# Kernel tuning notes

Measured on AMD Instinct MI355X. Metric: run time of the kernel, lower is better.

Reference implementation:

```python
import jax, jax.numpy as jnp
import numpy as np

INDIM = 1024
OUTDIM = 1024
NNZ = 65536  # expander pattern: avg degree 64 per output row
N = 50000


def setup_inputs() -> dict:
    key = jax.random.key(0)
    k1, k2, k3, k4, k5 = jax.random.split(key, 5)
    x = jax.random.normal(k1, (N, INDIM), dtype=jnp.float32)
    # glorot init for nnz values as in reset_parameters('glorot')
    stdv = np.sqrt(6.0 / (INDIM + OUTDIM))
    nnz_weight = jax.random.uniform(k2, (NNZ,), dtype=jnp.float32, minval=-stdv, maxval=stdv)
    bias = jax.random.normal(k3, (OUTDIM,), dtype=jnp.float32) * 0.02
    row = jax.random.randint(k4, (NNZ,), 0, OUTDIM, dtype=jnp.int64)
    col = jax.random.randint(k5, (NNZ,), 0, INDIM, dtype=jnp.int64)
    edge_index = jnp.stack([row, col])  # [2, NNZ]
    return {"x": x, "nnz_weight": nnz_weight, "bias": bias, "edge_index": edge_index}


def reference(x, nnz_weight, bias, edge_index):
    # SparseTensor(row, col, sizes=(outdim, indim), value=nnz_weight);
    # y = (W @ x^T)^T + bias  ==  x @ W^T + bias
    # Sparsity pattern is fixed & small (1024x1024): scatter values into a
    # dense weight then use a dense GEMM (duplicates accumulate, matching SpMM).
    row, col = edge_index[0], edge_index[1]
    W = jnp.zeros((OUTDIM, INDIM), dtype=nnz_weight.dtype).at[row, col].add(nnz_weight)
    return x @ W.T + bias  # [N, OUTDIM]
```

## Files before the change

kernel.cpp:

```cpp
#include <hip/hip_runtime.h>
#include <cstdint>

#define INDIM 1024
#define OUTDIM 1024
#define NNZ 65536
#define M_ROWS 50000

typedef __bf16 bf16x8 __attribute__((ext_vector_type(8)));
typedef float f32x4 __attribute__((ext_vector_type(4)));
typedef unsigned int u32x4 __attribute__((ext_vector_type(4)));

__global__ void scatter_w_kernel(const float* __restrict__ vals,
                                 const int* __restrict__ edge,
                                 float* __restrict__ Wf) {
    int e = blockIdx.x * blockDim.x + threadIdx.x;
    if (e < NNZ) {
        int r = edge[e];
        int c = edge[NNZ + e];
        atomicAdd(&Wf[r * INDIM + c], vals[e]);
    }
}

__global__ void cvt_w_kernel(const float* __restrict__ Wf,
                             unsigned short* __restrict__ Wb) {
    int i = blockIdx.x * blockDim.x + threadIdx.x;
    unsigned u = __builtin_bit_cast(unsigned, Wf[i]) + 0x8000u;
    Wb[i] = (unsigned short)(u >> 16);
}

__device__ __forceinline__ unsigned pack_bf16x2(float a, float b) {
    unsigned ua = __builtin_bit_cast(unsigned, a) + 0x8000u;
    unsigned ub = __builtin_bit_cast(unsigned, b) + 0x8000u;
    return (ua >> 16) | (ub & 0xffff0000u);
}

__device__ __forceinline__ void async_copy16(const void* g, void* l) {
    __builtin_amdgcn_global_load_lds(
        (const __attribute__((address_space(1))) void*)g,
        (__attribute__((address_space(3))) void*)l, 16, 0, 0);
}

__global__ void __launch_bounds__(256)
gemm_bt_kernel(const float* __restrict__ X,
               const unsigned short* __restrict__ Wb,
               const float* __restrict__ bias,
               float* __restrict__ out) {
    __shared__ unsigned As[128 * 16];
    __shared__ unsigned short Bs[128 * 32];

    const int t = threadIdx.x;
    const int w = t >> 6;
    const int l = t & 63;
    const int wr = w >> 1;
    const int wc = w & 1;
    const int quad = l >> 4;
    const int lr = l & 15;

    const int bid = blockIdx.x;
    int m_t, n_t;
    if (bid < 3072) {
        m_t = ((bid >> 6) << 3) + (bid & 7);
        n_t = (bid >> 3) & 7;
    } else {
        int r = bid - 3072;
        m_t = 384 + (r >> 3);
        n_t = r & 7;
    }
    const int m0 = m_t * 128;
    const int n0 = n_t * 128;

    const int ar  = t >> 1;
    const int ac0 = (t & 1) * 2;
    const int as_sw = (ar >> 1) & 3;
    int arow = m0 + ar;
    if (arow >= M_ROWS) arow = M_ROWS - 1;
    const float* aptr = X + (long)arow * INDIM + (t & 1) * 16;
    unsigned* as_row = &As[ar * 16];
    const int aph0 = (ac0 ^ as_sw) * 4;
    const int aph1 = ((ac0 + 1) ^ as_sw) * 4;

    f32x4 acc[4][4];
#pragma unroll
    for (int i = 0; i < 4; i++)
#pragma unroll
        for (int j = 0; j < 4; j++) acc[i][j] = (f32x4)0.0f;

    float biasv[4];
#pragma unroll
    for (int j = 0; j < 4; j++) biasv[j] = bias[n0 + wc * 64 + j * 16 + lr];

    int bsrc_off[2];
    int brow_[2];
#pragma unroll
    for (int i = 0; i < 2; i++) {
        int c_idx = i * 256 + t;
        int brow = c_idx >> 2;
        int pphys = c_idx & 3;
        int pdata = pphys ^ ((brow >> 1) & 3);
        brow_[i] = brow;
        bsrc_off[i] = pdata * 8;
    }

    for (int kt = 0; kt < INDIM; kt += 32) {
#pragma unroll
        for (int i = 0; i < 2; i++) {
            const unsigned short* g = Wb + (long)(n0 + brow_[i]) * INDIM + kt + bsrc_off[i];
            char* lbase = (char*)Bs + (size_t)(i * 256 + w * 64) * 16;
            async_copy16(g, lbase);
        }

        const float* ap = aptr + kt;
        f32x4 f0 = *(const f32x4*)(ap);
        f32x4 f1 = *(const f32x4*)(ap + 4);
        f32x4 f2 = *(const f32x4*)(ap + 8);
        f32x4 f3 = *(const f32x4*)(ap + 12);
        u32x4 p0, p1;
        p0.x = pack_bf16x2(f0.x, f0.y);
        p0.y = pack_bf16x2(f0.z, f0.w);
        p0.z = pack_bf16x2(f1.x, f1.y);
        p0.w = pack_bf16x2(f1.z, f1.w);
        p1.x = pack_bf16x2(f2.x, f2.y);
        p1.y = pack_bf16x2(f2.z, f2.w);
        p1.z = pack_bf16x2(f3.x, f3.y);
        p1.w = pack_bf16x2(f3.z, f3.w);
        *(u32x4*)(as_row + aph0) = p0;
        *(u32x4*)(as_row + aph1) = p1;

        __syncthreads();

        bf16x8 af[4], bf[4];
#pragma unroll
        for (int i = 0; i < 4; i++) {
            int row = wr * 64 + i * 16 + lr;
            int ph = quad ^ ((row >> 1) & 3);
            af[i] = *(const bf16x8*)((const unsigned short*)As + row * 32 + ph * 8);
        }
#pragma unroll
        for (int j = 0; j < 4; j++) {
            int row = wc * 64 + j * 16 + lr;
            int ph = quad ^ ((row >> 1) & 3);
            bf[j] = *(const bf16x8*)(Bs + row * 32 + ph * 8);
        }
#pragma unroll
        for (int i = 0; i < 4; i++)
#pragma unroll
            for (int j = 0; j < 4; j++)
                acc[i][j] = __builtin_amdgcn_mfma_f32_16x16x32_bf16(af[i], bf[j], acc[i][j], 0, 0, 0);

        __syncthreads();
    }

#pragma unroll
    for (int i = 0; i < 4; i++) {
#pragma unroll
        for (int j = 0; j < 4; j++) {
            int col = n0 + wc * 64 + j * 16 + lr;
#pragma unroll
            for (int r = 0; r < 4; r++) {
                int row = m0 + wr * 64 + i * 16 + quad * 4 + r;
                if (row < M_ROWS) {
                    out[(long)row * OUTDIM + col] = acc[i][j][r] + biasv[j];
                }
            }
        }
    }
}

extern "C" void kernel_launch(void* const* d_in, const int* in_sizes, int n_in,
                              void* d_out, int out_size, void* d_ws, size_t ws_size,
                              hipStream_t stream) {
    const float* x    = (const float*)d_in[0];
    const float* nnzw = (const float*)d_in[1];
    const float* bias = (const float*)d_in[2];
    const int* edge   = (const int*)d_in[3];
    float* out        = (float*)d_out;

    float* Wf         = (float*)d_ws;
    unsigned short* Wb = (unsigned short*)((char*)d_ws + (size_t)OUTDIM * INDIM * 4);

    hipMemsetAsync(Wf, 0, (size_t)OUTDIM * INDIM * sizeof(float), stream);

    scatter_w_kernel<<<NNZ / 256, 256, 0, stream>>>(nnzw, edge, Wf);
    cvt_w_kernel<<<(OUTDIM * INDIM) / 256, 256, 0, stream>>>(Wf, Wb);

    gemm_bt_kernel<<<dim3(3128), 256, 0, stream>>>(x, Wb, bias, out);
}
```

Baseline: 519.8 us.

## Pre-convert X to bf16 and stream both GEMM operands via async LDS loads

Adds a separate pass that converts the fp32 input X to bf16 in workspace memory. The GEMM then loads both A and B tiles with direct global-to-LDS async copies instead of doing per-tile fp32 loads, packing and LDS stores in registers. This removes repeated conversion work from the GEMM and halves the A-operand bytes it reads, and it sets a higher occupancy hint. The cost is an extra full pass that reads X once in fp32 and writes it back in bf16. The new path runs only when the workspace is large enough, otherwise the old kernel is used.

```diff
diff --git a/kernel.cpp b/kernel.cpp
--- a/kernel.cpp
+++ b/kernel.cpp
@@ -34,10 +34,124 @@
     return (ua >> 16) | (ub & 0xffff0000u);
 }
 
+__global__ void cvt_x_kernel(const float* __restrict__ X,
+                             unsigned short* __restrict__ Xb) {
+    long i = ((long)blockIdx.x * blockDim.x + threadIdx.x) * 8;
+    f32x4 a = *(const f32x4*)(X + i);
+    f32x4 b = *(const f32x4*)(X + i + 4);
+    u32x4 p;
+    p.x = pack_bf16x2(a.x, a.y);
+    p.y = pack_bf16x2(a.z, a.w);
+    p.z = pack_bf16x2(b.x, b.y);
+    p.w = pack_bf16x2(b.z, b.w);
+    *(u32x4*)(Xb + i) = p;
+}
+
 __device__ __forceinline__ void async_copy16(const void* g, void* l) {
     __builtin_amdgcn_global_load_lds(
         (const __attribute__((address_space(1))) void*)g,
         (__attribute__((address_space(3))) void*)l, 16, 0, 0);
+}
+
+__global__ void __launch_bounds__(256, 4)
+gemm_bb_kernel(const unsigned short* __restrict__ Xb,
+               const unsigned short* __restrict__ Wb,
+               const float* __restrict__ bias,
+               float* __restrict__ out) {
+    __shared__ unsigned short As[128 * 32];
+    __shared__ unsigned short Bs[128 * 32];
+
+    const int t = threadIdx.x;
+    const int w = t >> 6;
+    const int l = t & 63;
+    const int wr = w >> 1;
+    const int wc = w & 1;
+    const int quad = l >> 4;
+    const int lr = l & 15;
+
+    const int bid = blockIdx.x;
+    int m_t, n_t;
+    if (bid < 3072) {
+        m_t = ((bid >> 6) << 3) + (bid & 7);
+        n_t = (bid >> 3) & 7;
+    } else {
+        int r = bid - 3072;
+        m_t = 384 + (r >> 3);
+        n_t = r & 7;
+    }
+    const int m0 = m_t * 128;
+    const int n0 = n_t * 128;
+
+    int row_[2], soff_[2], arow_[2];
+#pragma unroll
+    for (int i = 0; i < 2; i++) {
+        int c_idx = i * 256 + t;
+        int row = c_idx >> 2;
+        int pphys = c_idx & 3;
+        int pdata = pphys ^ ((row >> 1) & 3);
+        row_[i] = row;
+        soff_[i] = pdata * 8;
+        int ar = m0 + row;
+        arow_[i] = (ar < M_ROWS) ? ar : (M_ROWS - 1);
+    }
+
+    f32x4 acc[4][4];
+#pragma unroll
+    for (int i = 0; i < 4; i++)
+#pragma unroll
+        for (int j = 0; j < 4; j++) acc[i][j] = (f32x4)0.0f;
+
+    float biasv[4];
+#pragma unroll
+    for (int j = 0; j < 4; j++) biasv[j] = bias[n0 + wc * 64 + j * 16 + lr];
+
+    for (int kt = 0; kt < INDIM; kt += 32) {
+#pragma unroll
+        for (int i = 0; i < 2; i++) {
+            async_copy16(Xb + (long)arow_[i] * INDIM + kt + soff_[i],
+                         (char*)As + (size_t)(i * 256 + w * 64) * 16);
+            async_copy16(Wb + (long)(n0 + row_[i]) * INDIM + kt + soff_[i],
+                         (char*)Bs + (size_t)(i * 256 + w * 64) * 16);
+        }
+
+        __syncthreads();
+
+        bf16x8 af[4], bfr[4];
+#pragma unroll
+        for (int i = 0; i < 4; i++) {
+            int row = wr * 64 + i * 16 + lr;
+            int ph = quad ^ ((row >> 1) & 3);
+            af[i] = *(const bf16x8*)(As + row * 32 + ph * 8);
+        }
+#pragma unroll
+        for (int j = 0; j < 4; j++) {
+            int row = wc * 64 + j * 16 + lr;
+            int ph = quad ^ ((row >> 1) & 3);
+            bfr[j] = *(const bf16x8*)(Bs + row * 32 + ph * 8);
+        }
+#pragma unroll
+        for (int i = 0; i < 4; i++)
+#pragma unroll
+            for (int j = 0; j < 4; j++)
+                acc[i][j] = __builtin_amdgcn_mfma_f32_16x16x32_bf16(af[i], bfr[j], acc[i][j], 0, 0, 0);
+
+        __syncthreads();
+    }
+
+#pragma unroll
+    for (int i = 0; i < 4; i++) {
+#pragma unroll
+        for (int j = 0; j < 4; j++) {
+            int col = n0 + wc * 64 + j * 16 + lr;
+#pragma unroll
+            for (int r = 0; r < 4; r++) {
+                int row = m0 + wr * 64 + i * 16 + quad * 4 + r;
+                if (row < M_ROWS) {
+                    out[(long)row * OUTDIM + col] = acc[i][j][r] + biasv[j];
+                }
+            }
+        }
+    }
 }
 
 __global__ void __launch_bounds__(256)
@@ -128,7 +242,7 @@
 
         __syncthreads();
 
-        bf16x8 af[4], bf[4];
+        bf16x8 af[4], bfr[4];
 #pragma unroll
         for (int i = 0; i < 4; i++) {
             int row = wr * 64 + i * 16 + lr;
@@ -139,13 +253,13 @@
         for (int j = 0; j < 4; j++) {
             int row = wc * 64 + j * 16 + lr;
             int ph = quad ^ ((row >> 1) & 3);
-            bf[j] = *(const bf16x8*)(Bs + row * 32 + ph * 8);
+            bfr[j] = *(const bf16x8*)(Bs + row * 32 + ph * 8);
         }
 #pragma unroll
         for (int i = 0; i < 4; i++)
 #pragma unroll
             for (int j = 0; j < 4; j++)
-                acc[i][j] = __builtin_amdgcn_mfma_f32_16x16x32_bf16(af[i], bf[j], acc[i][j], 0, 0, 0);
+                acc[i][j] = __builtin_amdgcn_mfma_f32_16x16x32_bf16(af[i], bfr[j], acc[i][j], 0, 0, 0);
 
         __syncthreads();
     }
@@ -175,13 +289,24 @@
     const int* edge   = (const int*)d_in[3];
     float* out        = (float*)d_out;
 
-    float* Wf         = (float*)d_ws;
-    unsigned short* Wb = (unsigned short*)((char*)d_ws + (size_t)OUTDIM * INDIM * 4);
-
-    hipMemsetAsync(Wf, 0, (size_t)OUTDIM * INDIM * sizeof(float), stream);
+    const size_t wf_bytes = (size_t)OUTDIM * INDIM * 4;
+    const size_t wb_bytes = (size_t)OUTDIM * INDIM * 2;
+    const size_t xb_off   = wf_bytes + wb_bytes;
+    const size_t xb_bytes = (size_t)M_ROWS * INDIM * 2;
+
+    float* Wf          = (float*)d_ws;
+    unsigned short* Wb = (unsigned short*)((char*)d_ws + wf_bytes);
+    unsigned short* Xb = (unsigned short*)((char*)d_ws + xb_off);
+
+    hipMemsetAsync(Wf, 0, wf_bytes, stream);
 
     scatter_w_kernel<<<NNZ / 256, 256, 0, stream>>>(nnzw, edge, Wf);
     cvt_w_kernel<<<(OUTDIM * INDIM) / 256, 256, 0, stream>>>(Wf, Wb);
 
-    gemm_bt_kernel<<<dim3(3128), 256, 0, stream>>>(x, Wb, bias, out);
-}
+    if (ws_size >= xb_off + xb_bytes) {
+        cvt_x_kernel<<<(M_ROWS * INDIM) / (256 * 8), 256, 0, stream>>>(x, Xb);
+        gemm_bb_kernel<<<dim3(3128), 256, 0, stream>>>(Xb, Wb, bias, out);
+    } else {
+        gemm_bt_kernel<<<dim3(3128), 256, 0, stream>>>(x, Wb, bias, out);
+    }
+}
```

Result: faster. 477.1 us (-8.2%).

## Double-buffer GEMM tiles with async fp32 A loads and convert on LDS read

Applied to the files above, without the earlier changes.

The GEMM main loop now double-buffers both operand tiles in LDS and prefetches the next k-tile with global_load_lds while the current one is computed. The fp32 A operand is copied straight into LDS with an XOR swizzle and converted to bf16 only when the fragments are read. This removes the synchronous register round-trip for X and lets global loads overlap the MFMA work. In exchange it doubles A's LDS footprint (fp32 storage plus two buffers, about 48KB per block), which may reduce occupancy, and it repeats the bf16 conversion for each wave that reads a fragment.

```diff
diff --git a/kernel.cpp b/kernel.cpp
--- a/kernel.cpp
+++ b/kernel.cpp
@@ -41,12 +41,12 @@
 }
 
 __global__ void __launch_bounds__(256)
-gemm_bt_kernel(const float* __restrict__ X,
-               const unsigned short* __restrict__ Wb,
-               const float* __restrict__ bias,
-               float* __restrict__ out) {
-    __shared__ unsigned As[128 * 16];
-    __shared__ unsigned short Bs[128 * 32];
+gemm_f32a_kernel(const float* __restrict__ X,
+                 const unsigned short* __restrict__ Wb,
+                 const float* __restrict__ bias,
+                 float* __restrict__ out) {
+    __shared__ float As[2][128 * 32];
+    __shared__ unsigned short Bs[2][128 * 32];
 
     const int t = threadIdx.x;
     const int w = t >> 6;
@@ -69,15 +69,33 @@
     const int m0 = m_t * 128;
     const int n0 = n_t * 128;
 
-    const int ar  = t >> 1;
-    const int ac0 = (t & 1) * 2;
-    const int as_sw = (ar >> 1) & 3;
-    int arow = m0 + ar;
-    if (arow >= M_ROWS) arow = M_ROWS - 1;
-    const float* aptr = X + (long)arow * INDIM + (t & 1) * 16;
-    unsigned* as_row = &As[ar * 16];
-    const int aph0 = (ac0 ^ as_sw) * 4;
-    const int aph1 = ((ac0 + 1) ^ as_sw) * 4;
+    const int ar0 = t >> 3;
+    const int apdata = (t & 7) ^ (ar0 & 7);
+    long asrc0, asrc1, asrc2, asrc3;
+    {
+        int r0 = m0 + ar0;
+        int r1 = m0 + ar0 + 32;
+        int r2 = m0 + ar0 + 64;
+        int r3 = m0 + ar0 + 96;
+        if (r0 >= M_ROWS) r0 = M_ROWS - 1;
+        if (r1 >= M_ROWS) r1 = M_ROWS - 1;
+        if (r2 >= M_ROWS) r2 = M_ROWS - 1;
+        if (r3 >= M_ROWS) r3 = M_ROWS - 1;
+        asrc0 = (long)r0 * INDIM + apdata * 4;
+        asrc1 = (long)r1 * INDIM + apdata * 4;
+        asrc2 = (long)r2 * INDIM + apdata * 4;
+        asrc3 = (long)r3 * INDIM + apdata * 4;
+    }
+
+    int brow0 = t >> 2;
+    int bsoff0 = ((t & 3) ^ ((brow0 >> 1) & 3)) * 8;
+    int brow1 = (256 + t) >> 2;
+    int bsoff1 = (((256 + t) & 3) ^ ((brow1 >> 1) & 3)) * 8;
+    const long bbase0 = (long)(n0 + brow0) * INDIM + bsoff0;
+    const long bbase1 = (long)(n0 + brow1) * INDIM + bsoff1;
+
+    const size_t aw = (size_t)(w * 64) * 16;
+    const size_t bw = (size_t)(w * 64) * 16;
 
     f32x4 acc[4][4];
 #pragma unroll
@@ -89,65 +107,63 @@
 #pragma unroll
     for (int j = 0; j < 4; j++) biasv[j] = bias[n0 + wc * 64 + j * 16 + lr];
 
-    int bsrc_off[2];
-    int brow_[2];
-#pragma unroll
-    for (int i = 0; i < 2; i++) {
-        int c_idx = i * 256 + t;
-        int brow = c_idx >> 2;
-        int pphys = c_idx & 3;
-        int pdata = pphys ^ ((brow >> 1) & 3);
-        brow_[i] = brow;
-        bsrc_off[i] = pdata * 8;
-    }
-
+    {
+        char* a = (char*)&As[0][0];
+        char* b = (char*)&Bs[0][0];
+        async_copy16(X + asrc0, a + aw);
+        async_copy16(X + asrc1, a + 4096 + aw);
+        async_copy16(X + asrc2, a + 8192 + aw);
+        async_copy16(X + asrc3, a + 12288 + aw);
+        async_copy16(Wb + bbase0, b + bw);
+        async_copy16(Wb + bbase1, b + 4096 + bw);
+    }
+    __syncthreads();
+
+    int buf = 0;
     for (int kt = 0; kt < INDIM; kt += 32) {
-#pragma unroll
-        for (int i = 0; i < 2; i++) {
-            const unsigned short* g = Wb + (long)(n0 + brow_[i]) * INDIM + kt + bsrc_off[i];
-            char* lbase = (char*)Bs + (size_t)(i * 256 + w * 64) * 16;
-            async_copy16(g, lbase);
-        }
-
-        const float* ap = aptr + kt;
-        f32x4 f0 = *(const f32x4*)(ap);
-        f32x4 f1 = *(const f32x4*)(ap + 4);
-        f32x4 f2 = *(const f32x4*)(ap + 8);
-        f32x4 f3 = *(const f32x4*)(ap + 12);
-        u32x4 p0, p1;
-        p0.x = pack_bf16x2(f0.x, f0.y);
-        p0.y = pack_bf16x2(f0.z, f0.w);
-        p0.z = pack_bf16x2(f1.x, f1.y);
-        p0.w = pack_bf16x2(f1.z, f1.w);
-        p1.x = pack_bf16x2(f2.x, f2.y);
-        p1.y = pack_bf16x2(f2.z, f2.w);
-        p1.z = pack_bf16x2(f3.x, f3.y);
-        p1.w = pack_bf16x2(f3.z, f3.w);
-        *(u32x4*)(as_row + aph0) = p0;
-        *(u32x4*)(as_row + aph1) = p1;
-
-        __syncthreads();
-
-        bf16x8 af[4], bf[4];
+        if (kt + 32 < INDIM) {
+            char* a = (char*)&As[buf ^ 1][0];
+            char* b = (char*)&Bs[buf ^ 1][0];
+            const int kn = kt + 32;
+            async_copy16(X + asrc0 + kn, a + aw);
+            async_copy16(X + asrc1 + kn, a + 4096 + aw);
+            async_copy16(X + asrc2 + kn, a + 8192 + aw);
+            async_copy16(X + asrc3 + kn, a + 12288 + aw);
+            async_copy16(Wb + bbase0 + kn, b + bw);
+            async_copy16(Wb + bbase1 + kn, b + 4096 + bw);
+        }
+
+        const float* As_c = &As[buf][0];
+        const unsigned short* Bs_c = &Bs[buf][0];
+        bf16x8 af[4], bfr[4];
+        const int p0 = (2 * quad) ^ (lr & 7);
 #pragma unroll
         for (int i = 0; i < 4; i++) {
             int row = wr * 64 + i * 16 + lr;
-            int ph = quad ^ ((row >> 1) & 3);
-            af[i] = *(const bf16x8*)((const unsigned short*)As + row * 32 + ph * 8);
+            const float* rp = As_c + row * 32;
+            f32x4 c0 = *(const f32x4*)(rp + p0 * 4);
+            f32x4 c1 = *(const f32x4*)(rp + (p0 ^ 1) * 4);
+            u32x4 u;
+            u.x = pack_bf16x2(c0.x, c0.y);
+            u.y = pack_bf16x2(c0.z, c0.w);
+            u.z = pack_bf16x2(c1.x, c1.y);
+            u.w = pack_bf16x2(c1.z, c1.w);
+            af[i] = __builtin_bit_cast(bf16x8, u);
         }
 #pragma unroll
         for (int j = 0; j < 4; j++) {
             int row = wc * 64 + j * 16 + lr;
             int ph = quad ^ ((row >> 1) & 3);
-            bf[j] = *(const bf16x8*)(Bs + row * 32 + ph * 8);
+            bfr[j] = *(const bf16x8*)(Bs_c + row * 32 + ph * 8);
         }
 #pragma unroll
         for (int i = 0; i < 4; i++)
 #pragma unroll
             for (int j = 0; j < 4; j++)
-                acc[i][j] = __builtin_amdgcn_mfma_f32_16x16x32_bf16(af[i], bf[j], acc[i][j], 0, 0, 0);
+                acc[i][j] = __builtin_amdgcn_mfma_f32_16x16x32_bf16(af[i], bfr[j], acc[i][j], 0, 0, 0);
 
         __syncthreads();
+        buf ^= 1;
     }
 
 #pragma unroll
@@ -175,13 +191,14 @@
     const int* edge   = (const int*)d_in[3];
     float* out        = (float*)d_out;
 
-    float* Wf         = (float*)d_ws;
-    unsigned short* Wb = (unsigned short*)((char*)d_ws + (size_t)OUTDIM * INDIM * 4);
-
-    hipMemsetAsync(Wf, 0, (size_t)OUTDIM * INDIM * sizeof(float), stream);
+    const size_t wf_bytes = (size_t)OUTDIM * INDIM * 4;
+    float* Wf          = (float*)d_ws;
+    unsigned short* Wb = (unsigned short*)((char*)d_ws + wf_bytes);
+
+    hipMemsetAsync(Wf, 0, wf_bytes, stream);
 
     scatter_w_kernel<<<NNZ / 256, 256, 0, stream>>>(nnzw, edge, Wf);
     cvt_w_kernel<<<(OUTDIM * INDIM) / 256, 256, 0, stream>>>(Wf, Wb);
 
-    gemm_bt_kernel<<<dim3(3128), 256, 0, stream>>>(x, Wb, bias, out);
-}
+    gemm_f32a_kernel<<<dim3(3128), 256, 0, stream>>>(x, Wb, bias, out);
+}
```

After: 506.6 us. 2.5% less time.
